# Kernel optimization log

Hardware: AMD Instinct MI355X
Metric: run time of the kernel (lower is better)

## Reference

```python
import jax, jax.numpy as jnp
import numpy as np

NUM_HEADS = 12
EPS = 1e-12  # torch F.normalize clamp_min eps


def _l2norm(t):
    return t / jnp.clip(jnp.linalg.norm(t, axis=-1, keepdims=True), EPS)


def setup_inputs() -> dict:
    key = jax.random.key(0)
    ks = jax.random.split(key, 6)
    B, N, C = 8, 4096, 768
    Nc, Nb, F = 1, 512, 16
    s = 0.02
    return {
        "x": jax.random.normal(ks[0], (B, N, C), jnp.float32),
        "bank": jax.random.normal(ks[1], (Nc, Nb, F), jnp.float32),
        "Wq": jax.random.normal(ks[2], (C, C), jnp.float32) * s,
        "Wkv": jax.random.normal(ks[3], (F, 2 * C), jnp.float32) * s,
        "Wlin": jax.random.normal(ks[4], (C, C), jnp.float32) * s,
        "b_lin": jnp.zeros((C,), jnp.float32),
        "prelu_a": jnp.asarray(0.25, jnp.float32),
        "temperature": jnp.ones((NUM_HEADS, 1, 1), jnp.float32),
    }


def reference(x, bank, Wq, Wkv, Wlin, b_lin, prelu_a, temperature):
    B, N, C = x.shape
    Nc, Nb, _ = bank.shape
    H = NUM_HEADS
    d = C // H
    # q: (B, H, N, d), L2-normalized along d
    q = _l2norm((x @ Wq).reshape(B, N, H, d).transpose(0, 2, 1, 3))
    # kv from (detached) bank: (2, Nc, H, Nb, d)
    kv = (bank @ Wkv).reshape(Nc, Nb, 2, H, d).transpose(2, 0, 3, 1, 4)
    k = _l2norm(kv[0])
    v = kv[1]
    # cosine attention with per-head learned temperature: (B, Nc, H, N, Nb)
    attn = jnp.einsum('bhnd,chmd->bchnm', q, k) * temperature
    attn = jax.nn.softmax(attn, axis=-1)
    # (dropout is identity in eval mode)
    out = jnp.einsum('bchnm,chmd->bchnd', attn, v)  # (B, Nc, H, N, d)
    out = out.reshape(B * Nc, H, N, d).transpose(0, 2, 1, 3).reshape(B, N, C)
    out = out @ Wlin + b_lin
    # PReLU with a single shared parameter
    return jnp.where(out >= 0, out, prelu_a * out)
```

## Files before the change

### kernel.cpp

```cpp
#include <hip/hip_runtime.h>
#include <cstdint>
#include <cstddef>

typedef unsigned short u16;
typedef __attribute__((ext_vector_type(8))) __bf16 bf16x8;
typedef __attribute__((ext_vector_type(4))) float f32x4;

#define MFMA(a, b, c) __builtin_amdgcn_mfma_f32_16x16x32_bf16(a, b, c, 0, 0, 0)

__device__ __forceinline__ u16 f2bf(float f) {
  union { float f; uint32_t u; } x; x.f = f;
  uint32_t r = x.u + 0x7fffu + ((x.u >> 16) & 1u);
  return (u16)(r >> 16);
}

__device__ __forceinline__ void gld16(const u16* g, u16* l) {
  __builtin_amdgcn_global_load_lds(
      (const __attribute__((address_space(1))) void*)g,
      (__attribute__((address_space(3))) void*)l, 16, 0, 0);
}

__global__ void cvt_f32_bf16(const float* __restrict__ src, u16* __restrict__ dst, int n4) {
  int i = blockIdx.x * blockDim.x + threadIdx.x;
  int stride = gridDim.x * blockDim.x;
  for (; i < n4; i += stride) {
    float4 v = ((const float4*)src)[i];
    ushort4 o;
    o.x = f2bf(v.x); o.y = f2bf(v.y); o.z = f2bf(v.z); o.w = f2bf(v.w);
    ((ushort4*)dst)[i] = o;
  }
}

__global__ void transpose_cvt(const float* __restrict__ src, u16* __restrict__ dst, int R, int C) {
  __shared__ float tile[32][33];
  int bx = blockIdx.x * 32, by = blockIdx.y * 32;
  int tx = threadIdx.x, ty = threadIdx.y;
  #pragma unroll
  for (int i = ty; i < 32; i += 8)
    tile[i][tx] = src[(size_t)(by + i) * C + bx + tx];
  __syncthreads();
  #pragma unroll
  for (int i = ty; i < 32; i += 8)
    dst[(size_t)(bx + i) * R + by + tx] = f2bf(tile[tx][i]);
}

__global__ void kv_prep(const float* __restrict__ bank, const float* __restrict__ Wkv,
                        const float* __restrict__ temp, u16* __restrict__ K, u16* __restrict__ VT) {
  int m = blockIdx.x & 511, h = blockIdx.x >> 9;
  int j = threadIdx.x;
  const float* br = bank + m * 16;
  float kj = 0.f, vj = 0.f;
  #pragma unroll
  for (int f = 0; f < 16; ++f) {
    float bv = br[f];
    kj = fmaf(bv, Wkv[f * 1536 + h * 64 + j], kj);
    vj = fmaf(bv, Wkv[f * 1536 + 768 + h * 64 + j], vj);
  }
  float ss = kj * kj;
  #pragma unroll
  for (int o = 32; o; o >>= 1) ss += __shfl_xor(ss, o);
  float rn = rsqrtf(fmaxf(ss, 1e-24f));
  K[((size_t)h * 512 + m) * 64 + j] = f2bf(kj * rn * temp[h] * 1.4426950408889634f);
  VT[((size_t)h * 64 + j) * 512 + m] = f2bf(vj);
}

template <int MODE>
__global__ __launch_bounds__(256, 3) void gemm_bt(
    const u16* __restrict__ A, const u16* __restrict__ BT, void* __restrict__ Cout,
    int M, int N, int K, const float* __restrict__ bias, const float* __restrict__ prelu) {
  __shared__ u16 sA[128 * 32];
  __shared__ u16 sB[128 * 32];
  const int ntiles = N >> 7;
  const int m0 = (blockIdx.x / ntiles) << 7;
  const int n0 = (blockIdx.x % ntiles) << 7;
  const int tid = threadIdx.x;
  const int w = tid >> 6, lane = tid & 63;
  const int wm = (w >> 1) << 6, wn = (w & 1) << 6;
  const int srow = lane >> 2, scol = (lane & 3) << 3;
  const u16* ga = A + (size_t)(m0 + (w << 5) + srow) * K + scol;
  const u16* gb = BT + (size_t)(n0 + (w << 5) + srow) * K + scol;
  u16* la = sA + (w << 5) * 32;
  u16* lb = sB + (w << 5) * 32;
  const int fr = lane & 15, fq = (lane >> 4) << 3;
  f32x4 acc[4][4] = {};

  for (int k0 = 0; k0 < K; k0 += 32) {
    __syncthreads();
    gld16(ga + k0, la);
    gld16(ga + k0 + (size_t)16 * K, la + 16 * 32);
    gld16(gb + k0, lb);
    gld16(gb + k0 + (size_t)16 * K, lb + 16 * 32);
    __syncthreads();
    bf16x8 af[4], bfr[4];
    #pragma unroll
    for (int t = 0; t < 4; ++t) {
      af[t] = *(const bf16x8*)(sA + (wm + t * 16 + fr) * 32 + fq);
      bfr[t] = *(const bf16x8*)(sB + (wn + t * 16 + fr) * 32 + fq);
    }
    #pragma unroll
    for (int i = 0; i < 4; ++i)
      #pragma unroll
      for (int j = 0; j < 4; ++j)
        acc[i][j] = MFMA(af[i], bfr[j], acc[i][j]);
  }

  const int q = lane >> 4;
  float a = (MODE == 1) ? prelu[0] : 0.f;
  #pragma unroll
  for (int tm = 0; tm < 4; ++tm)
    #pragma unroll
    for (int tn = 0; tn < 4; ++tn) {
      int col = n0 + wn + tn * 16 + fr;
      float bv = (MODE == 1) ? bias[col] : 0.f;
      #pragma unroll
      for (int r = 0; r < 4; ++r) {
        int row = m0 + wm + tm * 16 + q * 4 + r;
        float v = acc[tm][tn][r];
        if (MODE == 1) {
          v += bv;
          v = v >= 0.f ? v : v * a;
          ((float*)Cout)[(size_t)row * N + col] = v;
        } else {
          ((u16*)Cout)[(size_t)row * N + col] = f2bf(v);
        }
      }
    }
}

__global__ __launch_bounds__(512, 4) void attn_kern(
    const u16* __restrict__ Q, const u16* __restrict__ Kb,
    const u16* __restrict__ Vt, u16* __restrict__ O) {
  __shared__ __align__(16) u16 sK[2][64 * 72];
  __shared__ __align__(16) u16 sV[2][64 * 72];

  const int qb = blockIdx.x & 127;
  const int h = blockIdx.x >> 7;
  const int tid = threadIdx.x, w = tid >> 6, lane = tid & 63;
  const int fr = lane & 15, quad = lane >> 4;
  const int rowbase = qb * 256 + (w << 5);

  bf16x8 qa[2][2];
  #pragma unroll
  for (int g = 0; g < 2; ++g) {
    const u16* qp = Q + (size_t)(rowbase + g * 16 + fr) * 768 + h * 64 + (quad << 3);
    qa[g][0] = *(const bf16x8*)qp;
    qa[g][1] = *(const bf16x8*)(qp + 32);
    float ss = 0.f;
    #pragma unroll
    for (int j = 0; j < 8; ++j) {
      float f0 = (float)qa[g][0][j], f1 = (float)qa[g][1][j];
      ss += f0 * f0 + f1 * f1;
    }
    ss += __shfl_xor(ss, 16);
    ss += __shfl_xor(ss, 32);
    float rn = rsqrtf(fmaxf(ss, 1e-24f));
    #pragma unroll
    for (int j = 0; j < 8; ++j) {
      qa[g][0][j] = (__bf16)((float)qa[g][0][j] * rn);
      qa[g][1][j] = (__bf16)((float)qa[g][1][j] * rn);
    }
  }

  const u16* kg = Kb + (size_t)h * 512 * 64;
  const u16* vg = Vt + (size_t)h * 64 * 512;
  int4 kreg, vreg;
  auto load_chunk = [&](int c) {
    kreg = *(const int4*)(kg + (size_t)(c * 64 + (tid >> 3)) * 64 + (tid & 7) * 8);
    vreg = *(const int4*)(vg + (size_t)(tid >> 3) * 512 + c * 64 + (tid & 7) * 8);
  };
  auto store_chunk = [&](int buf) {
    *(int4*)(sK[buf] + (tid >> 3) * 72 + (tid & 7) * 8) = kreg;
    *(int4*)(sV[buf] + (tid >> 3) * 72 + (tid & 7) * 8) = vreg;
  };

  load_chunk(0);
  store_chunk(0);
  load_chunk(1);
  __syncthreads();

  f32x4 oa[2][4] = {};
  float ls[2] = {0.f, 0.f};

  for (int c = 0; c < 8; ++c) {
    const int cb = c & 1;
    if (c < 7) store_chunk((c + 1) & 1);
    if (c < 6) load_chunk(c + 2);

    #pragma unroll
    for (int ks = 0; ks < 2; ++ks) {
      f32x4 s[2][2];
      #pragma unroll
      for (int half = 0; half < 2; ++half) {
        const int mt = ks * 2 + half;
        const u16* kp = sK[cb] + (mt * 16 + fr) * 72 + (quad << 3);
        bf16x8 ak0 = *(const bf16x8*)kp;
        bf16x8 ak1 = *(const bf16x8*)(kp + 32);
        #pragma unroll
        for (int g = 0; g < 2; ++g) {
          f32x4 z = {0.f, 0.f, 0.f, 0.f};
          z = MFMA(ak0, qa[g][0], z);
          z = MFMA(ak1, qa[g][1], z);
          s[g][half] = z;
        }
      }
      bf16x8 pbf[2];
      #pragma unroll
      for (int g = 0; g < 2; ++g)
        #pragma unroll
        for (int half = 0; half < 2; ++half)
          #pragma unroll
          for (int r = 0; r < 4; ++r) {
            float p = __builtin_amdgcn_exp2f(s[g][half][r]);
            ls[g] += p;
            pbf[g][half * 4 + r] = (__bf16)p;
          }
      #pragma unroll
      for (int t = 0; t < 4; ++t) {
        const u16* vp = sV[cb] + (t * 16 + fr) * 72 + ks * 32 + (quad << 2);
        bf16x8 va;
        *(uint2*)&va = *(const uint2*)vp;
        *((uint2*)&va + 1) = *(const uint2*)(vp + 16);
        #pragma unroll
        for (int g = 0; g < 2; ++g)
          oa[g][t] = MFMA(va, pbf[g], oa[g][t]);
      }
    }
    __syncthreads();
  }

  #pragma unroll
  for (int g = 0; g < 2; ++g) {
    float l = ls[g];
    l += __shfl_xor(l, 16);
    l += __shfl_xor(l, 32);
    float rl = __builtin_amdgcn_rcpf(l);
    u16* op = O + (size_t)(rowbase + g * 16 + fr) * 768 + h * 64 + (quad << 2);
    #pragma unroll
    for (int t = 0; t < 4; ++t) {
      ushort4 pk;
      pk.x = f2bf(oa[g][t][0] * rl);
      pk.y = f2bf(oa[g][t][1] * rl);
      pk.z = f2bf(oa[g][t][2] * rl);
      pk.w = f2bf(oa[g][t][3] * rl);
      *(ushort4*)(op + t * 16) = pk;
    }
  }
}

extern "C" void kernel_launch(void* const* d_in, const int* in_sizes, int n_in,
                              void* d_out, int out_size, void* d_ws, size_t ws_size,
                              hipStream_t stream) {
  const float* x      = (const float*)d_in[0];
  const float* bank   = (const float*)d_in[1];
  const float* Wq     = (const float*)d_in[2];
  const float* Wkv    = (const float*)d_in[3];
  const float* Wlin   = (const float*)d_in[4];
  const float* b_lin  = (const float*)d_in[5];
  const float* prelu  = (const float*)d_in[6];
  const float* temp   = (const float*)d_in[7];
  float* out = (float*)d_out;

  char* ws = (char*)d_ws;
  const size_t NELEM = 25165824;
  u16* qbuf  = (u16*)ws;
  u16* xbuf  = (u16*)(ws + 50331648);
  u16* obuf  = xbuf;
  u16* wqt   = (u16*)(ws + 100663296);
  u16* wlt   = wqt + 589824;
  u16* kbuf  = wlt + 589824;
  u16* vtbuf = kbuf + 393216;

  cvt_f32_bf16<<<4096, 256, 0, stream>>>(x, xbuf, (int)(NELEM / 4));
  transpose_cvt<<<dim3(24, 24), dim3(32, 8), 0, stream>>>(Wq, wqt, 768, 768);
  transpose_cvt<<<dim3(24, 24), dim3(32, 8), 0, stream>>>(Wlin, wlt, 768, 768);
  kv_prep<<<6144, 64, 0, stream>>>(bank, Wkv, temp, kbuf, vtbuf);
  gemm_bt<0><<<1536, 256, 0, stream>>>(xbuf, wqt, qbuf, 32768, 768, 768, nullptr, nullptr);
  attn_kern<<<1536, 512, 0, stream>>>(qbuf, kbuf, vtbuf, obuf);
  gemm_bt<1><<<1536, 256, 0, stream>>>(obuf, wlt, out, 32768, 768, 768, b_lin, prelu);
}
```

Measured before the change: 395.1 us.

## Double-buffer LDS tiles in GEMM and swizzle block order

The GEMM kernel now uses two LDS buffers for the A and B tiles. It issues the global-to-LDS loads for the next k-step before computing on the current one, which removes one barrier per iteration and overlaps memory latency with MFMA work. Block indices are also remapped with a stride-8 swizzle to change which tiles run concurrently, aiming for better L2 reuse. LDS use doubles to 32KB per block, which may lower occupancy. The swizzle assumes the grid size is divisible by 8.

```diff
diff --git a/kernel.cpp b/kernel.cpp
--- a/kernel.cpp
+++ b/kernel.cpp
@@ -68,40 +68,47 @@
 __global__ __launch_bounds__(256, 3) void gemm_bt(
     const u16* __restrict__ A, const u16* __restrict__ BT, void* __restrict__ Cout,
     int M, int N, int K, const float* __restrict__ bias, const float* __restrict__ prelu) {
-  __shared__ u16 sA[128 * 32];
-  __shared__ u16 sB[128 * 32];
+  __shared__ u16 sA[2][128 * 32];
+  __shared__ u16 sB[2][128 * 32];
   const int ntiles = N >> 7;
-  const int m0 = (blockIdx.x / ntiles) << 7;
-  const int n0 = (blockIdx.x % ntiles) << 7;
+  const int swz = (blockIdx.x & 7) * (gridDim.x >> 3) + (blockIdx.x >> 3);
+  const int m0 = (swz / ntiles) << 7;
+  const int n0 = (swz % ntiles) << 7;
   const int tid = threadIdx.x;
   const int w = tid >> 6, lane = tid & 63;
   const int wm = (w >> 1) << 6, wn = (w & 1) << 6;
   const int srow = lane >> 2, scol = (lane & 3) << 3;
   const u16* ga = A + (size_t)(m0 + (w << 5) + srow) * K + scol;
   const u16* gb = BT + (size_t)(n0 + (w << 5) + srow) * K + scol;
-  u16* la = sA + (w << 5) * 32;
-  u16* lb = sB + (w << 5) * 32;
+  const int lofs = (w << 5) * 32;
   const int fr = lane & 15, fq = (lane >> 4) << 3;
   f32x4 acc[4][4] = {};
 
+  auto stage = [&](int buf, int k0) {
+    gld16(ga + k0, sA[buf] + lofs);
+    gld16(ga + k0 + (size_t)16 * K, sA[buf] + lofs + 16 * 32);
+    gld16(gb + k0, sB[buf] + lofs);
+    gld16(gb + k0 + (size_t)16 * K, sB[buf] + lofs + 16 * 32);
+  };
+
+  stage(0, 0);
+  __syncthreads();
+  int cur = 0;
   for (int k0 = 0; k0 < K; k0 += 32) {
-    __syncthreads();
-    gld16(ga + k0, la);
-    gld16(ga + k0 + (size_t)16 * K, la + 16 * 32);
-    gld16(gb + k0, lb);
-    gld16(gb + k0 + (size_t)16 * K, lb + 16 * 32);
-    __syncthreads();
+    if (k0 + 32 < K) stage(cur ^ 1, k0 + 32);
     bf16x8 af[4], bfr[4];
     #pragma unroll
     for (int t = 0; t < 4; ++t) {
-      af[t] = *(const bf16x8*)(sA + (wm + t * 16 + fr) * 32 + fq);
-      bfr[t] = *(const bf16x8*)(sB + (wn + t * 16 + fr) * 32 + fq);
+      af[t] = *(const bf16x8*)(sA[cur] + (wm + t * 16 + fr) * 32 + fq);
+      bfr[t] = *(const bf16x8*)(sB[cur] + (wn + t * 16 + fr) * 32 + fq);
     }
     #pragma unroll
     for (int i = 0; i < 4; ++i)
       #pragma unroll
       for (int j = 0; j < 4; ++j)
         acc[i][j] = MFMA(af[i], bfr[j], acc[i][j]);
+    __syncthreads();
+    cur ^= 1;
   }
 
   const int q = lane >> 4;
```

Result: faster. 370.3 us (-6.3%).
